# Optimization experiments

Hardware: AMD Instinct MI355X
Metric: run time of the kernel (lower is better)

Reference implementation:

```python
import jax, jax.numpy as jnp
import numpy as np

DIM = 768
HEADS = 12
HD = DIM // HEADS  # 64
WIN = 14
N = WIN * WIN  # 196
MLP_HID = 3072
EPS = 1e-6
SCALE = HD ** -0.5


def _ln(x, g, b):
    m = jnp.mean(x, axis=-1, keepdims=True)
    v = jnp.mean(jnp.square(x - m), axis=-1, keepdims=True)
    return (x - m) * jax.lax.rsqrt(v + EPS) * g + b


def _rel_table(rel):
    coords = jnp.arange(WIN)[:, None] - jnp.arange(WIN)[None, :] + (WIN - 1)
    return rel[coords]


def _window_partition(x, ws):
    B, H, W, C = x.shape
    pad_h = (ws - H % ws) % ws
    pad_w = (ws - W % ws) % ws
    x = jnp.pad(x, ((0, 0), (0, pad_h), (0, pad_w), (0, 0)))
    Hp, Wp = H + pad_h, W + pad_w
    x = x.reshape(B, Hp // ws, ws, Wp // ws, ws, C)
    win = x.transpose(0, 1, 3, 2, 4, 5).reshape(-1, ws, ws, C)
    return win, (Hp, Wp)


def _window_unpartition(win, ws, pad_hw, hw):
    Hp, Wp = pad_hw
    H, W = hw
    B = win.shape[0] // (Hp * Wp // ws // ws)
    x = win.reshape(B, Hp // ws, Wp // ws, ws, ws, -1)
    x = x.transpose(0, 1, 3, 2, 4, 5).reshape(B, Hp, Wp, -1)
    return x[:, :H, :W, :]


def _attention(x, qkv_w, qkv_b, proj_w, proj_b, rel_pos_h, rel_pos_w):
    Bw = x.shape[0]
    qkv = x.reshape(Bw, N, DIM) @ qkv_w + qkv_b  # (Bw, N, 3*DIM)
    qkv = qkv.reshape(Bw, N, 3, HEADS, HD).transpose(2, 0, 3, 1, 4)
    qkv = qkv.reshape(3, Bw * HEADS, N, HD)
    q, k, v = qkv[0], qkv[1], qkv[2]
    attn = jnp.einsum('bnd,bmd->bnm', q * SCALE, k)  # (Bw*H, N, N)
    Rh = _rel_table(rel_pos_h)
    Rw = _rel_table(rel_pos_w)
    r_q = q.reshape(-1, WIN, WIN, HD)
    rel_h = jnp.einsum('bhwc,hkc->bhwk', r_q, Rh)
    rel_w = jnp.einsum('bhwc,wkc->bhwk', r_q, Rw)
    attn = (attn.reshape(-1, WIN, WIN, WIN, WIN)
            + rel_h[:, :, :, :, None]
            + rel_w[:, :, :, None, :]).reshape(-1, N, N)
    attn = jax.nn.softmax(attn, axis=-1)
    out = jnp.einsum('bnm,bmd->bnd', attn, v)
    out = out.reshape(Bw, HEADS, WIN, WIN, HD).transpose(0, 2, 3, 1, 4)
    out = out.reshape(Bw, WIN, WIN, DIM)
    return out @ proj_w + proj_b


def setup_inputs() -> dict:
    key = jax.random.key(0)
    ks = jax.random.split(key, 10)
    s = 0.02
    return {
        'x': jax.random.normal(ks[0], (2, 64, 64, DIM), jnp.float32),
        'ln1_g': jnp.ones((DIM,), jnp.float32),
        'ln1_b': jnp.zeros((DIM,), jnp.float32),
        'qkv_w': jax.random.normal(ks[1], (DIM, 3 * DIM), jnp.float32) * s,
        'qkv_b': jax.random.normal(ks[2], (3 * DIM,), jnp.float32) * s,
        'proj_w': jax.random.normal(ks[3], (DIM, DIM), jnp.float32) * s,
        'proj_b': jax.random.normal(ks[4], (DIM,), jnp.float32) * s,
        'rel_pos_h': jax.random.normal(ks[5], (2 * WIN - 1, HD), jnp.float32) * s,
        'rel_pos_w': jax.random.normal(ks[6], (2 * WIN - 1, HD), jnp.float32) * s,
        'ln2_g': jnp.ones((DIM,), jnp.float32),
        'ln2_b': jnp.zeros((DIM,), jnp.float32),
        'fc1_w': jax.random.normal(ks[7], (DIM, MLP_HID), jnp.float32) * s,
        'fc1_b': jnp.zeros((MLP_HID,), jnp.float32),
        'fc2_w': jax.random.normal(ks[8], (MLP_HID, DIM), jnp.float32) * s,
        'fc2_b': jnp.zeros((DIM,), jnp.float32),
    }


def reference(x, ln1_g, ln1_b, qkv_w, qkv_b, proj_w, proj_b,
              rel_pos_h, rel_pos_w, ln2_g, ln2_b, fc1_w, fc1_b, fc2_w, fc2_b):
    B, H, W, _ = x.shape
    shortcut = x
    h = _ln(x, ln1_g, ln1_b)
    win, pad_hw = _window_partition(h, WIN)
    win = _attention(win, qkv_w, qkv_b, proj_w, proj_b, rel_pos_h, rel_pos_w)
    h = _window_unpartition(win, WIN, pad_hw, (H, W))
    x = shortcut + h  # drop_path prob 0 -> identity
    h = _ln(x, ln2_g, ln2_b)
    h = jax.nn.gelu(h @ fc1_w + fc1_b, approximate=False) @ fc2_w + fc2_b
    return x + h
```

## Files before the change

kernel.cpp:

```cpp
#include <hip/hip_runtime.h>
#include <hip/hip_bf16.h>
#include <math.h>


#define DIMC 768
#define HEADS 12
#define WIN 14
#define NTOK 196
#define NWIN 50
#define MROWS 9800
#define YROWS 8192
#define MLP_HID 3072

using bf16x8 = __attribute__((ext_vector_type(8))) short;
using f32x4  = __attribute__((ext_vector_type(4))) float;

__device__ __forceinline__ float bf2f(unsigned short u) {
    return __uint_as_float(((unsigned)u) << 16);
}
__device__ __forceinline__ unsigned short f2bf(float f) {
    unsigned u = __float_as_uint(f);
    unsigned r = (u + 0x7fffu + ((u >> 16) & 1u)) >> 16;
    return (unsigned short)r;
}
__device__ __forceinline__ void gl2lds16(const unsigned short* g, unsigned short* l) {
    __builtin_amdgcn_global_load_lds(
        (const __attribute__((address_space(1))) void*)g,
        (__attribute__((address_space(3))) void*)l, 16, 0, 0);
}

__device__ __forceinline__ float fast_gelu(float v) {
    float u = v * 0.70710678118654752f;
    float a = fabsf(u);
    float t = __builtin_amdgcn_rcpf(fmaf(0.3275911f, a, 1.0f));
    float p = t * fmaf(t, fmaf(t, fmaf(t, fmaf(t, 1.061405429f, -1.453152027f),
                       1.421413741f), -0.284496736f), 0.254829592f);
    float e = __expf(-u * u);
    float er = fmaf(-p, e, 1.0f);
    er = copysignf(er, v);
    return 0.5f * v * (1.0f + er);
}

__global__ __launch_bounds__(256) void transpose_all(
        const float* __restrict__ Wq, unsigned short* __restrict__ Tq,
        const float* __restrict__ Wp, unsigned short* __restrict__ Tp,
        const float* __restrict__ W1, unsigned short* __restrict__ T1,
        const float* __restrict__ W2, unsigned short* __restrict__ T2) {
    int id = blockIdx.x;
    const float* W; unsigned short* Wt; int K, N, nbx, rel;
    if (id < 432)       { W = Wq; Wt = Tq; K = 768;  N = 2304; nbx = 36; rel = id; }
    else if (id < 576)  { W = Wp; Wt = Tp; K = 768;  N = 768;  nbx = 12; rel = id - 432; }
    else if (id < 1152) { W = W1; Wt = T1; K = 768;  N = 3072; nbx = 48; rel = id - 576; }
    else                { W = W2; Wt = T2; K = 3072; N = 768;  nbx = 12; rel = id - 1152; }
    int bx = rel % nbx, by = rel / nbx;
    __shared__ float t[64][65];
    int k0 = by << 6, n0 = bx << 6;
    int tn = threadIdx.x & 63;
    int tk = threadIdx.x >> 6;
    #pragma unroll
    for (int r = 0; r < 16; r++) {
        int k = tk + r * 4;
        t[k][tn] = W[(size_t)(k0 + k) * N + n0 + tn];
    }
    __syncthreads();
    #pragma unroll
    for (int r = 0; r < 16; r++) {
        int n = tk + r * 4;
        Wt[(size_t)(n0 + n) * K + k0 + tn] = f2bf(t[tn][n]);
    }
}

__global__ __launch_bounds__(256) void ln1_win_kernel(
        const float* __restrict__ x, const float* __restrict__ g,
        const float* __restrict__ b, unsigned short* __restrict__ h1) {
    int tid = threadIdx.x;
    int row = blockIdx.x * 4 + (tid >> 6);
    int lane = tid & 63;
    if (row >= MROWS) return;
    int w = row / NTOK, t = row % NTOK;
    int bi = w / 25, wr = w % 25;
    int gy = (wr / 5) * WIN + t / WIN;
    int gx = (wr % 5) * WIN + t % WIN;
    unsigned short* out = h1 + (size_t)row * DIMC;
    if (gy >= 64 || gx >= 64) {
        #pragma unroll
        for (int j = 0; j < 12; j++) out[lane + 64 * j] = 0;
        return;
    }
    const float* xr = x + ((size_t)((bi * 64 + gy) * 64 + gx)) * DIMC;
    float v[12], s = 0.f;
    #pragma unroll
    for (int j = 0; j < 12; j++) { v[j] = xr[lane + 64 * j]; s += v[j]; }
    #pragma unroll
    for (int o = 32; o > 0; o >>= 1) s += __shfl_xor(s, o);
    float mean = s * (1.f / 768.f);
    float q = 0.f;
    #pragma unroll
    for (int j = 0; j < 12; j++) { float d = v[j] - mean; q += d * d; }
    #pragma unroll
    for (int o = 32; o > 0; o >>= 1) q += __shfl_xor(q, o);
    float inv = rsqrtf(q * (1.f / 768.f) + 1e-6f);
    #pragma unroll
    for (int j = 0; j < 12; j++) {
        int c = lane + 64 * j;
        out[c] = f2bf((v[j] - mean) * inv * g[c] + b[c]);
    }
}

__global__ __launch_bounds__(256) void ln2_kernel(
        const float* __restrict__ y, const float* __restrict__ g,
        const float* __restrict__ b, unsigned short* __restrict__ h2) {
    int tid = threadIdx.x;
    int row = blockIdx.x * 4 + (tid >> 6);
    int lane = tid & 63;
    const float* xr = y + (size_t)row * DIMC;
    float v[12], s = 0.f;
    #pragma unroll
    for (int j = 0; j < 12; j++) { v[j] = xr[lane + 64 * j]; s += v[j]; }
    #pragma unroll
    for (int o = 32; o > 0; o >>= 1) s += __shfl_xor(s, o);
    float mean = s * (1.f / 768.f);
    float q = 0.f;
    #pragma unroll
    for (int j = 0; j < 12; j++) { float d = v[j] - mean; q += d * d; }
    #pragma unroll
    for (int o = 32; o > 0; o >>= 1) q += __shfl_xor(q, o);
    float inv = rsqrtf(q * (1.f / 768.f) + 1e-6f);
    unsigned short* out = h2 + (size_t)row * DIMC;
    #pragma unroll
    for (int j = 0; j < 12; j++) {
        int c = lane + 64 * j;
        out[c] = f2bf((v[j] - mean) * inv * g[c] + b[c]);
    }
}

__global__ __launch_bounds__(256) void build_aug(
        const unsigned short* __restrict__ qkvb,
        const float* __restrict__ relph, const float* __restrict__ relpw,
        unsigned short* __restrict__ Aaug, unsigned short* __restrict__ Vt) {
    __shared__ unsigned short qs[208 * 72];
    __shared__ unsigned short rt[64 * 72];
    int tid = threadIdx.x;
    int bh = blockIdx.x, w = bh / HEADS, head = bh % HEADS;
    int lane = tid & 63, wave = tid >> 6;
    int l15 = lane & 15, q4 = lane >> 4, q8 = q4 * 8;
    size_t base = (size_t)w * NTOK * 2304 + head * 64;
    unsigned short* ab = Aaug + (size_t)bh * 256 * 96;

    for (int e = tid; e < 196 * 8; e += 256) {
        int t = e >> 3, s8 = (e & 7) * 8;
        bf16x8 qv = *(const bf16x8*)&qkvb[base + (size_t)t * 2304 + s8];
        *(bf16x8*)&qs[t * 72 + s8] = qv;
        *(bf16x8*)&ab[t * 96 + s8] = qv;
    }
    for (int e = tid; e < 12 * 8; e += 256) {
        bf16x8 z = {};
        *(bf16x8*)&qs[(196 + (e >> 3)) * 72 + (e & 7) * 8] = z;
    }
    for (int e = tid; e < 64 * 8; e += 256) {
        int r = e >> 3, s8 = (e & 7) * 8;
        bf16x8 ov = {};
        if (r < 54) {
            const float* src = (r < 27 ? relph + (size_t)r * 64
                                       : relpw + (size_t)(r - 27) * 64) + s8;
            #pragma unroll
            for (int jj = 0; jj < 8; jj++) ov[jj] = (short)f2bf(src[jj]);
        }
        *(bf16x8*)&rt[r * 72 + s8] = ov;
    }
    for (int e = tid; e < 60 * 12; e += 256) {
        bf16x8 z = {};
        *(bf16x8*)&ab[(size_t)(196 + e / 12) * 96 + (e % 12) * 8] = z;
    }
    for (int e = tid; e < 196; e += 256) {
        ab[e * 96 + 92] = 0; ab[e * 96 + 93] = 0;
        ab[e * 96 + 94] = 0; ab[e * 96 + 95] = 0;
    }
    __syncthreads();

    #pragma unroll
    for (int t = 0; t < 4; t++) {
        int it = wave * 4 + t;
        if (it >= 13) break;
        bf16x8 a0 = *(bf16x8*)&qs[(it * 16 + l15) * 72 + q8];
        bf16x8 a1 = *(bf16x8*)&qs[(it * 16 + l15) * 72 + 32 + q8];
        #pragma unroll
        for (int rt4 = 0; rt4 < 4; rt4++) {
            bf16x8 b0 = *(bf16x8*)&rt[(rt4 * 16 + l15) * 72 + q8];
            bf16x8 b1 = *(bf16x8*)&rt[(rt4 * 16 + l15) * 72 + 32 + q8];
            f32x4 d4 = {};
            d4 = __builtin_amdgcn_mfma_f32_16x16x32_bf16(a0, b0, d4, 0, 0, 0);
            d4 = __builtin_amdgcn_mfma_f32_16x16x32_bf16(a1, b1, d4, 0, 0, 0);
            int rcol = rt4 * 16 + l15;
            #pragma unroll
            for (int r = 0; r < 4; r++) {
                int i = it * 16 + q4 * 4 + r;
                if (i < 196 && rcol < 54) {
                    if (rcol < 27) {
                        int c = 13 + i / 14 - rcol;
                        if (c >= 0 && c < 14) ab[i * 96 + 64 + c] = f2bf(d4[r]);
                    } else {
                        int c = 13 + i % 14 - (rcol - 27);
                        if (c >= 0 && c < 14) ab[i * 96 + 78 + c] = f2bf(d4[r]);
                    }
                }
            }
        }
    }

    unsigned short* vtb = Vt + (size_t)bh * 64 * 224;
    for (int e = tid; e < 196 * 8; e += 256) {
        int j = e >> 3, dg = (e & 7) * 8;
        bf16x8 vv = *(const bf16x8*)&qkvb[base + 1536 + (size_t)j * 2304 + dg];
        #pragma unroll
        for (int k = 0; k < 8; k++)
            vtb[(size_t)(dg + k) * 224 + j] = (unsigned short)vv[k];
    }
    for (int e = tid; e < 64 * 28; e += 256)
        vtb[(size_t)(e / 28) * 224 + 196 + (e % 28)] = 0;
}

__global__ __launch_bounds__(256) void attn_mfma(
        const unsigned short* __restrict__ qkvb,
        const unsigned short* __restrict__ Aaug,
        const unsigned short* __restrict__ Vt,
        unsigned short* __restrict__ out) {
    __shared__ unsigned short Kls[208 * 96];
    __shared__ unsigned short Pls[4][64 * 40];
    int tid = threadIdx.x;
    int bh = blockIdx.x, w = bh / HEADS, head = bh % HEADS;
    int wave = tid >> 6, lane = tid & 63;
    int l15 = lane & 15, q4 = lane >> 4, q8 = q4 * 8;
    size_t kbase = (size_t)w * NTOK * 2304 + head * 64 + 768;
    for (int e = tid; e < 196 * 8; e += 256) {
        int t = e >> 3, s8 = (e & 7) * 8;
        bf16x8 kv = *(const bf16x8*)&qkvb[kbase + (size_t)t * 2304 + s8];
        bf16x8 ko;
        #pragma unroll
        for (int jj = 0; jj < 8; jj++)
            ko[jj] = (short)f2bf(bf2f((unsigned short)kv[jj]) * 0.125f);
        *(bf16x8*)&Kls[t * 96 + s8] = ko;
    }
    bf16x8 z8 = {};
    for (int e = tid; e < 208 * 4; e += 256)
        *(bf16x8*)&Kls[(e >> 2) * 96 + 64 + (e & 3) * 8] = z8;
    for (int e = tid; e < 12 * 8; e += 256)
        *(bf16x8*)&Kls[(196 + (e >> 3)) * 96 + (e & 7) * 8] = z8;
    __syncthreads();
    for (int e = tid; e < 196; e += 256) {
        Kls[e * 96 + 64 + e / WIN] = 0x3F80;
        Kls[e * 96 + 78 + e % WIN] = 0x3F80;
    }
    bf16x8 af[4][3];
    const unsigned short* abse = Aaug + (size_t)bh * 256 * 96;
    #pragma unroll
    for (int it = 0; it < 4; it++)
        #pragma unroll
        for (int c = 0; c < 3; c++)
            af[it][c] = *(const bf16x8*)&abse[(size_t)(wave * 64 + it * 16 + l15) * 96 + c * 32 + q8];
    __syncthreads();

    const unsigned short* vtb = Vt + (size_t)bh * 64 * 224;
    f32x4 o[4][4] = {};
    float lacc[4][4] = {{0.f}};
    bf16x8 bv[4];
    #pragma unroll
    for (int dt = 0; dt < 4; dt++)
        bv[dt] = *(const bf16x8*)&vtb[(dt * 16 + l15) * 224 + q8];

    for (int jp = 0; jp < 7; jp++) {
        f32x4 s[4][2] = {};
        #pragma unroll
        for (int half = 0; half < 2; half++) {
            int jt = jp * 2 + half;
            if (jt < 13) {
                #pragma unroll
                for (int c = 0; c < 3; c++) {
                    bf16x8 bk = *(bf16x8*)&Kls[(jt * 16 + l15) * 96 + c * 32 + q8];
                    #pragma unroll
                    for (int it = 0; it < 4; it++)
                        s[it][half] = __builtin_amdgcn_mfma_f32_16x16x32_bf16(
                            af[it][c], bk, s[it][half], 0, 0, 0);
                }
            }
        }
        __syncthreads();
        #pragma unroll
        for (int half = 0; half < 2; half++) {
            int jt = jp * 2 + half;
            bool valid = (jt < 13) && (jt * 16 + l15) < 196;
            #pragma unroll
            for (int it = 0; it < 4; it++)
                #pragma unroll
                for (int r = 0; r < 4; r++) {
                    float p = valid ? __expf(s[it][half][r]) : 0.f;
                    unsigned short pb = f2bf(p);
                    lacc[it][r] += bf2f(pb);
                    Pls[wave][(it * 16 + q4 * 4 + r) * 40 + half * 16 + l15] = pb;
                }
        }
        __syncthreads();
        bf16x8 ap[4];
        #pragma unroll
        for (int it = 0; it < 4; it++)
            ap[it] = *(bf16x8*)&Pls[wave][(it * 16 + l15) * 40 + q8];
        bf16x8 bvn[4];
        if (jp < 6) {
            #pragma unroll
            for (int dt = 0; dt < 4; dt++)
                bvn[dt] = *(const bf16x8*)&vtb[(dt * 16 + l15) * 224 + (jp + 1) * 32 + q8];
        }
        #pragma unroll
        for (int dt = 0; dt < 4; dt++)
            #pragma unroll
            for (int it = 0; it < 4; it++)
                o[it][dt] = __builtin_amdgcn_mfma_f32_16x16x32_bf16(
                    ap[it], bv[dt], o[it][dt], 0, 0, 0);
        if (jp < 6) {
            #pragma unroll
            for (int dt = 0; dt < 4; dt++) bv[dt] = bvn[dt];
        }
    }
    #pragma unroll
    for (int it = 0; it < 4; it++)
        #pragma unroll
        for (int r = 0; r < 4; r++) {
            float v = lacc[it][r];
            v += __shfl_xor(v, 1); v += __shfl_xor(v, 2);
            v += __shfl_xor(v, 4); v += __shfl_xor(v, 8);
            lacc[it][r] = 1.f / v;
        }
    #pragma unroll
    for (int it = 0; it < 4; it++) {
        int i0 = wave * 64 + it * 16 + q4 * 4;
        #pragma unroll
        for (int r = 0; r < 4; r++) {
            if (i0 + r < 196) {
                size_t rowb = (size_t)(w * NTOK + i0 + r) * DIMC + head * 64;
                #pragma unroll
                for (int dt = 0; dt < 4; dt++)
                    out[rowb + dt * 16 + l15] = f2bf(o[it][dt][r] * lacc[it][r]);
            }
        }
    }
}

template <int EPI, int BN>
__global__ __launch_bounds__(256) void mgemm(
        const unsigned short* __restrict__ A, const unsigned short* __restrict__ Bt,
        const float* __restrict__ bias, void* __restrict__ Cout,
        const float* __restrict__ resid, int M, int Nn, int K,
        int nbx, int nby) {
    const int NI = BN / 32;
    __shared__ unsigned short As[2][128 * 32];
    __shared__ unsigned short Bs[2][BN * 32];
    int tid = threadIdx.x;
    int lane = tid & 63, wave = tid >> 6;
    int l15 = lane & 15, q4 = lane >> 4;
    int xq8 = (q4 ^ ((l15 >> 1) & 3)) * 8;
    int id = blockIdx.x;
    int per = nbx * 8;
    int s = id / per;
    int rem = id - s * per;
    int rmax = nby - s * 8; if (rmax > 8) rmax = 8;
    int bx = rem / rmax;
    int r_ = rem - bx * rmax;
    int by = s * 8 + r_;
    int m0 = by << 7, n0 = bx * BN;
    int wm = (wave >> 1) * 64, wn = (wave & 1) * (BN / 2);
    int srow0 = wave * 32 + (lane >> 2);
    int srow1 = srow0 + 16;
    int sseg = ((lane & 3) ^ ((lane >> 3) & 3)) * 8;
    int rmA0 = m0 + srow0; if (rmA0 >= M) rmA0 = M - 1;
    int rmA1 = m0 + srow1; if (rmA1 >= M) rmA1 = M - 1;
    const unsigned short* gA0 = A + (size_t)rmA0 * K + sseg;
    const unsigned short* gA1 = A + (size_t)rmA1 * K + sseg;
    int browB = (BN == 128) ? srow0 : (wave * 16 + (lane >> 2));
    const unsigned short* gB0 = Bt + (size_t)(n0 + browB) * K + sseg;
    const unsigned short* gB1 = Bt + (size_t)(n0 + srow1) * K + sseg;
    int lofsA = wave * 1024 + lane * 8;
    int lofsB = ((BN == 128) ? wave * 1024 : wave * 512) + lane * 8;
    f32x4 acc[4][NI] = {};
    gl2lds16(gA0, &As[0][lofsA]);
    gl2lds16(gA1, &As[0][lofsA + 512]);
    gl2lds16(gB0, &Bs[0][lofsB]);
    if (BN == 128) gl2lds16(gB1, &Bs[0][lofsB + 512]);
    int cur = 0;
    for (int k0 = 0; k0 < K; k0 += 32) {
        __syncthreads();
        int kn = k0 + 32;
        if (kn < K) {
            gl2lds16(gA0 + kn, &As[cur ^ 1][lofsA]);
            gl2lds16(gA1 + kn, &As[cur ^ 1][lofsA + 512]);
            gl2lds16(gB0 + kn, &Bs[cur ^ 1][lofsB]);
            if (BN == 128) gl2lds16(gB1 + kn, &Bs[cur ^ 1][lofsB + 512]);
        }
        bf16x8 bfr[NI];
        #pragma unroll
        for (int ni = 0; ni < NI; ni++)
            bfr[ni] = *(bf16x8*)&Bs[cur][(wn + ni * 16 + l15) * 32 + xq8];
        #pragma unroll
        for (int mi = 0; mi < 4; mi++) {
            bf16x8 afr = *(bf16x8*)&As[cur][(wm + mi * 16 + l15) * 32 + xq8];
            #pragma unroll
            for (int ni = 0; ni < NI; ni++)
                acc[mi][ni] = __builtin_amdgcn_mfma_f32_16x16x32_bf16(
                    afr, bfr[ni], acc[mi][ni], 0, 0, 0);
        }
        cur ^= 1;
    }
    int q4r = (lane >> 4) * 4;
    #pragma unroll
    for (int mi = 0; mi < 4; mi++) {
        #pragma unroll
        for (int r = 0; r < 4; r++) {
            int row = m0 + wm + mi * 16 + q4r + r;
            if (row >= M) continue;
            if (EPI == 2) {
                int w = row / NTOK, t = row % NTOK;
                int bi = w / 25, wr = w % 25;
                int gy = (wr / 5) * WIN + t / WIN;
                int gx = (wr % 5) * WIN + t % WIN;
                if (gy >= 64 || gx >= 64) continue;
                size_t orow = ((size_t)((bi * 64 + gy) * 64 + gx)) * DIMC;
                #pragma unroll
                for (int ni = 0; ni < NI; ni++) {
                    int col = n0 + wn + ni * 16 + l15;
                    float v = acc[mi][ni][r] + bias[col];
                    ((float*)Cout)[orow + col] = resid[orow + col] + v;
                }
            } else {
                #pragma unroll
                for (int ni = 0; ni < NI; ni++) {
                    int col = n0 + wn + ni * 16 + l15;
                    float v = acc[mi][ni][r] + bias[col];
                    if (EPI == 0) {
                        ((unsigned short*)Cout)[(size_t)row * Nn + col] = f2bf(v);
                    } else if (EPI == 1) {
                        v = fast_gelu(v);
                        ((unsigned short*)Cout)[(size_t)row * Nn + col] = f2bf(v);
                    } else {
                        ((float*)Cout)[(size_t)row * Nn + col] =
                            resid[(size_t)row * Nn + col] + v;
                    }
                }
            }
        }
    }
}

extern "C" void kernel_launch(void* const* d_in, const int* in_sizes, int n_in,
                              void* d_out, int out_size, void* d_ws, size_t ws_size,
                              hipStream_t stream) {
    const float* x      = (const float*)d_in[0];
    const float* ln1_g  = (const float*)d_in[1];
    const float* ln1_b  = (const float*)d_in[2];
    const float* qkv_w  = (const float*)d_in[3];
    const float* qkv_b  = (const float*)d_in[4];
    const float* proj_w = (const float*)d_in[5];
    const float* proj_b = (const float*)d_in[6];
    const float* rel_h  = (const float*)d_in[7];
    const float* rel_w  = (const float*)d_in[8];
    const float* ln2_g  = (const float*)d_in[9];
    const float* ln2_b  = (const float*)d_in[10];
    const float* fc1_w  = (const float*)d_in[11];
    const float* fc1_b  = (const float*)d_in[12];
    const float* fc2_w  = (const float*)d_in[13];
    const float* fc2_b  = (const float*)d_in[14];
    float* out = (float*)d_out;
    char* ws = (char*)d_ws;

    unsigned short* wt_qkv  = (unsigned short*)(ws);
    unsigned short* wt_proj = (unsigned short*)(ws + 3538944);
    unsigned short* wt_fc1  = (unsigned short*)(ws + 4718592);
    unsigned short* wt_fc2  = (unsigned short*)(ws + 9437184);
    unsigned short* qkvb    = (unsigned short*)(ws + 14155776);
    float*          yb      = (float*)        (ws + 14155776);
    unsigned short* h2      = (unsigned short*)(ws + 39321600);
    unsigned short* h1      = (unsigned short*)(ws + 59314176);
    unsigned short* attn_o  = h1;
    unsigned short* zb      = h1;
    unsigned short* Aaug    = (unsigned short*)(ws + 74366976);
    unsigned short* Vt      = (unsigned short*)(ws + 103858176);

    transpose_all<<<1728, 256, 0, stream>>>(
        qkv_w, wt_qkv, proj_w, wt_proj, fc1_w, wt_fc1, fc2_w, wt_fc2);

    ln1_win_kernel<<<(MROWS + 3) / 4, 256, 0, stream>>>(x, ln1_g, ln1_b, h1);

    mgemm<0, 128><<<18 * 77, 256, 0, stream>>>(
        h1, wt_qkv, qkv_b, qkvb, nullptr, MROWS, 2304, DIMC, 18, 77);

    build_aug<<<NWIN * HEADS, 256, 0, stream>>>(qkvb, rel_h, rel_w, Aaug, Vt);

    attn_mfma<<<NWIN * HEADS, 256, 0, stream>>>(qkvb, Aaug, Vt, attn_o);

    mgemm<2, 64><<<12 * 77, 256, 0, stream>>>(
        attn_o, wt_proj, proj_b, yb, x, MROWS, DIMC, DIMC, 12, 77);

    ln2_kernel<<<YROWS / 4, 256, 0, stream>>>(yb, ln2_g, ln2_b, h2);

    mgemm<1, 128><<<24 * 64, 256, 0, stream>>>(
        h2, wt_fc1, fc1_b, zb, nullptr, YROWS, MLP_HID, DIMC, 24, 64);

    mgemm<3, 64><<<12 * 64, 256, 0, stream>>>(
        zb, wt_fc2, fc2_b, out, yb, YROWS, DIMC, MLP_HID, 12, 64);
}
```

Baseline: 438.6 us.

## Triple-buffer GEMM LDS tiles with explicit vmcnt waits for two-stage prefetch

Moves the shared GEMM kernel from double to triple buffering of the A/B LDS tiles and issues global-to-LDS loads two k-steps ahead. A partial s_waitcnt vmcnt now waits only for the current tile, followed by a raw s_barrier, instead of a full __syncthreads. The aim is to hide more global-load latency behind MFMA work. In exchange it uses 1.5x the LDS, which may lower occupancy, and it relies on the hand-counted vmcnt value matching the number of loads issued per stage.

```diff
diff --git a/kernel.cpp b/kernel.cpp
--- a/kernel.cpp
+++ b/kernel.cpp
@@ -352,8 +352,9 @@
         const float* __restrict__ resid, int M, int Nn, int K,
         int nbx, int nby) {
     const int NI = BN / 32;
-    __shared__ unsigned short As[2][128 * 32];
-    __shared__ unsigned short Bs[2][BN * 32];
+    constexpr int LPT = (BN == 128) ? 4 : 3;
+    __shared__ unsigned short As[3][128 * 32];
+    __shared__ unsigned short Bs[3][BN * 32];
     int tid = threadIdx.x;
     int lane = tid & 63, wave = tid >> 6;
     int l15 = lane & 15, q4 = lane >> 4;
@@ -381,19 +382,32 @@
     int lofsA = wave * 1024 + lane * 8;
     int lofsB = ((BN == 128) ? wave * 1024 : wave * 512) + lane * 8;
     f32x4 acc[4][NI] = {};
+    int nt = K >> 5;
     gl2lds16(gA0, &As[0][lofsA]);
     gl2lds16(gA1, &As[0][lofsA + 512]);
     gl2lds16(gB0, &Bs[0][lofsB]);
     if (BN == 128) gl2lds16(gB1, &Bs[0][lofsB + 512]);
+    if (nt > 1) {
+        gl2lds16(gA0 + 32, &As[1][lofsA]);
+        gl2lds16(gA1 + 32, &As[1][lofsA + 512]);
+        gl2lds16(gB0 + 32, &Bs[1][lofsB]);
+        if (BN == 128) gl2lds16(gB1 + 32, &Bs[1][lofsB + 512]);
+    }
     int cur = 0;
-    for (int k0 = 0; k0 < K; k0 += 32) {
-        __syncthreads();
-        int kn = k0 + 32;
-        if (kn < K) {
-            gl2lds16(gA0 + kn, &As[cur ^ 1][lofsA]);
-            gl2lds16(gA1 + kn, &As[cur ^ 1][lofsA + 512]);
-            gl2lds16(gB0 + kn, &Bs[cur ^ 1][lofsB]);
-            if (BN == 128) gl2lds16(gB1 + kn, &Bs[cur ^ 1][lofsB + 512]);
+    for (int t = 0; t < nt; ++t) {
+        if (t + 1 < nt) {
+            asm volatile("s_waitcnt vmcnt(%0)" :: "i"(LPT) : "memory");
+        } else {
+            asm volatile("s_waitcnt vmcnt(0)" ::: "memory");
+        }
+        __builtin_amdgcn_s_barrier();
+        if (t + 2 < nt) {
+            int b2 = cur + 2; if (b2 >= 3) b2 -= 3;
+            int kn = (t + 2) << 5;
+            gl2lds16(gA0 + kn, &As[b2][lofsA]);
+            gl2lds16(gA1 + kn, &As[b2][lofsA + 512]);
+            gl2lds16(gB0 + kn, &Bs[b2][lofsB]);
+            if (BN == 128) gl2lds16(gB1 + kn, &Bs[b2][lofsB + 512]);
         }
         bf16x8 bfr[NI];
         #pragma unroll
@@ -407,7 +421,7 @@
                 acc[mi][ni] = __builtin_amdgcn_mfma_f32_16x16x32_bf16(
                     afr, bfr[ni], acc[mi][ni], 0, 0, 0);
         }
-        cur ^= 1;
+        cur = (cur == 2) ? 0 : cur + 1;
     }
     int q4r = (lane >> 4) * 4;
     #pragma unroll
```

Result: faster. 428.7 us (-2.3%).

## Enlarge GEMM tiles to 256x128 with 512-thread blocks and explicit vmcnt barrier

Applied to the files above, without the earlier changes.

Every GEMM now uses a single 256x128 output tile computed by 8 waves in a 512-thread block, replacing the 128x128 and 128x64 variants. Each block loads one A/B tile per k-step, which raises operand reuse and cuts global traffic per flop. The plain __syncthreads is replaced by an explicit vmcnt(0) wait plus s_barrier. In exchange the grids get much smaller (for example 192 blocks for fc2 and 234 for proj), which may leave CUs idle or cause wave-quantization tails on a 256-CU part.

```diff
diff --git a/kernel.cpp b/kernel.cpp
--- a/kernel.cpp
+++ b/kernel.cpp
@@ -345,15 +345,14 @@
     }
 }
 
-template <int EPI, int BN>
-__global__ __launch_bounds__(256) void mgemm(
+template <int EPI>
+__global__ __launch_bounds__(512) void mgemm(
         const unsigned short* __restrict__ A, const unsigned short* __restrict__ Bt,
         const float* __restrict__ bias, void* __restrict__ Cout,
         const float* __restrict__ resid, int M, int Nn, int K,
         int nbx, int nby) {
-    const int NI = BN / 32;
-    __shared__ unsigned short As[2][128 * 32];
-    __shared__ unsigned short Bs[2][BN * 32];
+    __shared__ unsigned short As[2][256 * 32];
+    __shared__ unsigned short Bs[2][128 * 32];
     int tid = threadIdx.x;
     int lane = tid & 63, wave = tid >> 6;
     int l15 = lane & 15, q4 = lane >> 4;
@@ -366,44 +365,40 @@
     int bx = rem / rmax;
     int r_ = rem - bx * rmax;
     int by = s * 8 + r_;
-    int m0 = by << 7, n0 = bx * BN;
-    int wm = (wave >> 1) * 64, wn = (wave & 1) * (BN / 2);
-    int srow0 = wave * 32 + (lane >> 2);
-    int srow1 = srow0 + 16;
-    int sseg = ((lane & 3) ^ ((lane >> 3) & 3)) * 8;
-    int rmA0 = m0 + srow0; if (rmA0 >= M) rmA0 = M - 1;
-    int rmA1 = m0 + srow1; if (rmA1 >= M) rmA1 = M - 1;
+    int m0 = by << 8, n0 = bx << 7;
+    int wm = (wave >> 1) * 64, wn = (wave & 1) * 64;
+    int srow = tid >> 2;
+    int sseg = ((tid & 3) ^ ((tid >> 3) & 3)) * 8;
+    int rmA0 = m0 + srow;       if (rmA0 >= M) rmA0 = M - 1;
+    int rmA1 = m0 + 128 + srow; if (rmA1 >= M) rmA1 = M - 1;
     const unsigned short* gA0 = A + (size_t)rmA0 * K + sseg;
     const unsigned short* gA1 = A + (size_t)rmA1 * K + sseg;
-    int browB = (BN == 128) ? srow0 : (wave * 16 + (lane >> 2));
-    const unsigned short* gB0 = Bt + (size_t)(n0 + browB) * K + sseg;
-    const unsigned short* gB1 = Bt + (size_t)(n0 + srow1) * K + sseg;
-    int lofsA = wave * 1024 + lane * 8;
-    int lofsB = ((BN == 128) ? wave * 1024 : wave * 512) + lane * 8;
-    f32x4 acc[4][NI] = {};
-    gl2lds16(gA0, &As[0][lofsA]);
-    gl2lds16(gA1, &As[0][lofsA + 512]);
-    gl2lds16(gB0, &Bs[0][lofsB]);
-    if (BN == 128) gl2lds16(gB1, &Bs[0][lofsB + 512]);
+    const unsigned short* gB0 = Bt + (size_t)(n0 + srow) * K + sseg;
+    int lofs = tid * 8;
+    f32x4 acc[4][4] = {};
+    int nt = K >> 5;
+    gl2lds16(gA0, &As[0][lofs]);
+    gl2lds16(gA1, &As[0][4096 + lofs]);
+    gl2lds16(gB0, &Bs[0][lofs]);
     int cur = 0;
-    for (int k0 = 0; k0 < K; k0 += 32) {
-        __syncthreads();
-        int kn = k0 + 32;
-        if (kn < K) {
-            gl2lds16(gA0 + kn, &As[cur ^ 1][lofsA]);
-            gl2lds16(gA1 + kn, &As[cur ^ 1][lofsA + 512]);
-            gl2lds16(gB0 + kn, &Bs[cur ^ 1][lofsB]);
-            if (BN == 128) gl2lds16(gB1 + kn, &Bs[cur ^ 1][lofsB + 512]);
-        }
-        bf16x8 bfr[NI];
-        #pragma unroll
-        for (int ni = 0; ni < NI; ni++)
+    for (int t = 0; t < nt; ++t) {
+        asm volatile("s_waitcnt vmcnt(0)" ::: "memory");
+        __builtin_amdgcn_s_barrier();
+        if (t + 1 < nt) {
+            int kn = (t + 1) << 5;
+            gl2lds16(gA0 + kn, &As[cur ^ 1][lofs]);
+            gl2lds16(gA1 + kn, &As[cur ^ 1][4096 + lofs]);
+            gl2lds16(gB0 + kn, &Bs[cur ^ 1][lofs]);
+        }
+        bf16x8 bfr[4];
+        #pragma unroll
+        for (int ni = 0; ni < 4; ni++)
             bfr[ni] = *(bf16x8*)&Bs[cur][(wn + ni * 16 + l15) * 32 + xq8];
         #pragma unroll
         for (int mi = 0; mi < 4; mi++) {
             bf16x8 afr = *(bf16x8*)&As[cur][(wm + mi * 16 + l15) * 32 + xq8];
             #pragma unroll
-            for (int ni = 0; ni < NI; ni++)
+            for (int ni = 0; ni < 4; ni++)
                 acc[mi][ni] = __builtin_amdgcn_mfma_f32_16x16x32_bf16(
                     afr, bfr[ni], acc[mi][ni], 0, 0, 0);
         }
@@ -424,14 +419,14 @@
                 if (gy >= 64 || gx >= 64) continue;
                 size_t orow = ((size_t)((bi * 64 + gy) * 64 + gx)) * DIMC;
                 #pragma unroll
-                for (int ni = 0; ni < NI; ni++) {
+                for (int ni = 0; ni < 4; ni++) {
                     int col = n0 + wn + ni * 16 + l15;
                     float v = acc[mi][ni][r] + bias[col];
                     ((float*)Cout)[orow + col] = resid[orow + col] + v;
                 }
             } else {
                 #pragma unroll
-                for (int ni = 0; ni < NI; ni++) {
+                for (int ni = 0; ni < 4; ni++) {
                     int col = n0 + wn + ni * 16 + l15;
                     float v = acc[mi][ni][r] + bias[col];
                     if (EPI == 0) {
@@ -488,21 +483,21 @@
 
     ln1_win_kernel<<<(MROWS + 3) / 4, 256, 0, stream>>>(x, ln1_g, ln1_b, h1);
 
-    mgemm<0, 128><<<18 * 77, 256, 0, stream>>>(
-        h1, wt_qkv, qkv_b, qkvb, nullptr, MROWS, 2304, DIMC, 18, 77);
+    mgemm<0><<<18 * 39, 512, 0, stream>>>(
+        h1, wt_qkv, qkv_b, qkvb, nullptr, MROWS, 2304, DIMC, 18, 39);
 
     build_aug<<<NWIN * HEADS, 256, 0, stream>>>(qkvb, rel_h, rel_w, Aaug, Vt);
 
     attn_mfma<<<NWIN * HEADS, 256, 0, stream>>>(qkvb, Aaug, Vt, attn_o);
 
-    mgemm<2, 64><<<12 * 77, 256, 0, stream>>>(
-        attn_o, wt_proj, proj_b, yb, x, MROWS, DIMC, DIMC, 12, 77);
+    mgemm<2><<<6 * 39, 512, 0, stream>>>(
+        attn_o, wt_proj, proj_b, yb, x, MROWS, DIMC, DIMC, 6, 39);
 
     ln2_kernel<<<YROWS / 4, 256, 0, stream>>>(yb, ln2_g, ln2_b, h2);
 
-    mgemm<1, 128><<<24 * 64, 256, 0, stream>>>(
-        h2, wt_fc1, fc1_b, zb, nullptr, YROWS, MLP_HID, DIMC, 24, 64);
-
-    mgemm<3, 64><<<12 * 64, 256, 0, stream>>>(
-        zb, wt_fc2, fc2_b, out, yb, YROWS, DIMC, MLP_HID, 12, 64);
-}
+    mgemm<1><<<24 * 32, 512, 0, stream>>>(
+        h2, wt_fc1, fc1_b, zb, nullptr, YROWS, MLP_HID, DIMC, 24, 32);
+
+    mgemm<3><<<6 * 32, 512, 0, stream>>>(
+        zb, wt_fc2, fc2_b, out, yb, YROWS, DIMC, MLP_HID, 6, 32);
+}
```

After: 433.2 us. Within noise of the previous version (-1.2%).
